# Optimization experiments

Hardware: AMD Instinct MI355X
Metric: run time of the kernel (lower is better)

## Reference

```python
import jax, jax.numpy as jnp
import numpy as np

N_ATOMS = 1_000_000
N_IN = 128
N_HID = 64
N_MOL = 25_000


def setup_inputs() -> dict:
    key = jax.random.key(0)
    k1, k2, k3, k4 = jax.random.split(key, 4)
    x = jax.random.normal(k1, (N_ATOMS, N_IN), dtype=jnp.float32)
    W1 = jax.random.normal(k2, (N_IN, N_HID), dtype=jnp.float32) * (1.0 / np.sqrt(N_IN))
    b1 = jnp.zeros((N_HID,), dtype=jnp.float32)
    W2 = jax.random.normal(k3, (N_HID, 1), dtype=jnp.float32) * (1.0 / np.sqrt(N_HID))
    b2 = jnp.zeros((1,), dtype=jnp.float32)
    idx_m = jnp.sort(jax.random.randint(k4, (N_ATOMS,), 0, N_MOL, dtype=jnp.int32))
    return {"x": x, "W1": W1, "b1": b1, "W2": W2, "b2": b2,
            "idx_m": idx_m, "num_segments": N_MOL}


def reference(x, W1, b1, W2, b2, idx_m, num_segments):
    # Atomwise MLP: Dense(silu) -> Dense(linear), per-atom output [N, 1]
    h = jax.nn.silu(x @ W1 + b1)            # [N, 64]
    y_atom = h @ W2 + b2                    # [N, 1]
    # scatter_add over molecule ids, then squeeze last dim
    y = jax.ops.segment_sum(y_atom, idx_m, num_segments=num_segments)  # [M, 1]
    y = jnp.squeeze(y, -1)                  # [M]
    return y
```

## Files before the change

### kernel.cpp

```cpp
#include <hip/hip_runtime.h>
#include <hip/hip_bf16.h>

typedef __attribute__((ext_vector_type(8))) short bf16x8;
typedef __attribute__((ext_vector_type(4))) short s16x4;
typedef __attribute__((ext_vector_type(4))) float f32x4;
typedef __attribute__((ext_vector_type(4))) int   i32x4;

#define N_IN  128
#define N_HID 64
#define LDS_PAD 8
#define TPB 256
#define WAVES_PER_BLOCK 4

static __device__ inline short f2bf(float f) {
    unsigned u = __float_as_uint(f);
    u += 0x7fffu + ((u >> 16) & 1u);
    return (short)(u >> 16);
}

static __device__ inline bf16x8 cvt8(f32x4 lo, f32x4 hi) {
    int i0, i1, i2, i3;
    asm("v_cvt_pk_bf16_f32 %0, %1, %2" : "=v"(i0) : "v"(lo[0]), "v"(lo[1]));
    asm("v_cvt_pk_bf16_f32 %0, %1, %2" : "=v"(i1) : "v"(lo[2]), "v"(lo[3]));
    asm("v_cvt_pk_bf16_f32 %0, %1, %2" : "=v"(i2) : "v"(hi[0]), "v"(hi[1]));
    asm("v_cvt_pk_bf16_f32 %0, %1, %2" : "=v"(i3) : "v"(hi[2]), "v"(hi[3]));
    i32x4 w = {i0, i1, i2, i3};
    return __builtin_bit_cast(bf16x8, w);
}


__global__ __launch_bounds__(TPB, 3)
void atomwise_mfma_kernel(const float* __restrict__ x,
                          const float* __restrict__ W1,
                          const float* __restrict__ b1,
                          const float* __restrict__ W2,
                          const float* __restrict__ b2,
                          const int*   __restrict__ idx_m,
                          float*       __restrict__ out,
                          int n_atoms)
{
    __shared__ short w1t[N_HID][N_IN + LDS_PAD];

    const int tid = threadIdx.x;

    for (int e = tid; e < N_IN * N_HID; e += TPB) {
        int k = e >> 6;
        int n = e & 63;
        w1t[n][k] = f2bf(W1[e]);
    }
    __syncthreads();

    const int lane = tid & 63;
    const int wv   = tid >> 6;
    const int l15  = lane & 15;
    const int g    = lane >> 4;

    bf16x8 bfrag[4][4];
    #pragma unroll
    for (int kt = 0; kt < 4; ++kt)
        #pragma unroll
        for (int nt = 0; nt < 4; ++nt) {
            const short* rp = &w1t[nt * 16 + l15][kt * 32 + g * 4];
            s16x4 q0 = *reinterpret_cast<const s16x4*>(rp);
            s16x4 q1 = *reinterpret_cast<const s16x4*>(rp + 16);
            bf16x8 b;
            b[0] = q0[0]; b[1] = q0[1]; b[2] = q0[2]; b[3] = q0[3];
            b[4] = q1[0]; b[5] = q1[1]; b[6] = q1[2]; b[7] = q1[3];
            bfrag[kt][nt] = b;
        }

    float bb[4], w2v[4];
    #pragma unroll
    for (int nt = 0; nt < 4; ++nt) {
        bb[nt]  = b1[nt * 16 + l15];
        w2v[nt] = W2[nt * 16 + l15];
    }
    const float b2v = b2[0];

    const int n_tiles = (n_atoms + 15) >> 4;
    const int n_waves = gridDim.x * WAVES_PER_BLOCK;
    int tile = blockIdx.x * WAVES_PER_BLOCK + wv;
    if (tile >= n_tiles) return;

    f32x4 xf[8];
    int mv;
    {
        int row  = tile * 16 + l15;
        int rowc = row < n_atoms ? row : (n_atoms - 1);
        const float* xp = x + (size_t)rowc * N_IN + g * 4;
        #pragma unroll
        for (int j = 0; j < 8; ++j)
            xf[j] = *reinterpret_cast<const f32x4*>(xp + j * 16);
        mv = idx_m[rowc];
    }

    while (true) {
        bf16x8 a[4];
        #pragma unroll
        for (int kt = 0; kt < 4; ++kt)
            a[kt] = cvt8(xf[2 * kt], xf[2 * kt + 1]);

        const int  ntile     = tile + n_waves;
        const bool have_next = ntile < n_tiles;
        int nmv = 0;
        if (have_next) {
            int row  = ntile * 16 + l15;
            int rowc = row < n_atoms ? row : (n_atoms - 1);
            const float* xp = x + (size_t)rowc * N_IN + g * 4;
            #pragma unroll
            for (int j = 0; j < 8; ++j)
                xf[j] = *reinterpret_cast<const f32x4*>(xp + j * 16);
            nmv = idx_m[rowc];
        }

        f32x4 acc[4] = {};
        #pragma unroll
        for (int kt = 0; kt < 4; ++kt)
            #pragma unroll
            for (int nt = 0; nt < 4; ++nt)
                acc[nt] = __builtin_amdgcn_mfma_f32_16x16x32_bf16(
                              a[kt], bfrag[kt][nt], acc[nt], 0, 0, 0);

        float p[4];
        #pragma unroll
        for (int j = 0; j < 4; ++j) {
            float s = 0.f;
            #pragma unroll
            for (int nt = 0; nt < 4; ++nt) {
                float z = acc[nt][j] + bb[nt];
                float e = __expf(-z);
                float h = z * __builtin_amdgcn_rcpf(1.f + e);
                s += h * w2v[nt];
            }
            p[j] = s;
        }

        const int  first = __shfl(mv, 0);
        const bool full  = (tile * 16 + 16) <= n_atoms;
        const bool uni   = full && (__all(mv == first) != 0);

        if (uni) {
            float s = p[0] + p[1] + p[2] + p[3];
            #pragma unroll
            for (int m = 1; m < 64; m <<= 1)
                s += __shfl_xor(s, m, 64);
            if (lane == 0)
                atomicAdd(&out[first], s + 16.0f * b2v);
        } else {
            int ia[4];
            #pragma unroll
            for (int j = 0; j < 4; ++j)
                ia[j] = __shfl(mv, g * 4 + j);
            #pragma unroll
            for (int m = 1; m < 16; m <<= 1) {
                #pragma unroll
                for (int j = 0; j < 4; ++j)
                    p[j] += __shfl_xor(p[j], m, 64);
            }
            if (l15 == 0) {
                #pragma unroll
                for (int j = 0; j < 4; ++j) {
                    int atom = tile * 16 + g * 4 + j;
                    if (atom < n_atoms)
                        atomicAdd(&out[ia[j]], p[j] + b2v);
                }
            }
        }

        if (!have_next) break;
        tile = ntile;
        mv   = nmv;
    }
}

extern "C" void kernel_launch(void* const* d_in, const int* in_sizes, int n_in,
                              void* d_out, int out_size, void* d_ws, size_t ws_size,
                              hipStream_t stream) {
    const float* x   = (const float*)d_in[0];
    const float* W1  = (const float*)d_in[1];
    const float* b1  = (const float*)d_in[2];
    const float* W2  = (const float*)d_in[3];
    const float* b2  = (const float*)d_in[4];
    const int*   idx = (const int*)d_in[5];

    const int n_atoms = in_sizes[0] / N_IN;
    float* out = (float*)d_out;

    hipMemsetAsync(d_out, 0, (size_t)out_size * sizeof(float), stream);

    const int blocks = 2048;
    atomwise_mfma_kernel<<<blocks, TPB, 0, stream>>>(
        x, W1, b1, W2, b2, idx, out, n_atoms);
}
```

Before: 113.2 us.

## Double-buffer x tile prefetch with two interleaved tiles per wave

Each wave now keeps two independent tiles in flight (A and B), prefetching the tile two steps ahead for each buffer, so more global loads are outstanding while MFMA and the epilogue run. The epilogue is factored into a helper. The launch-bounds occupancy hint drops from 3 to 2 to give room for the extra register buffers. This trades fewer resident waves for more memory-level parallelism per wave.

Measured after the change: 117.2 us. 3.6% more time.

```diff
diff --git a/kernel.cpp b/kernel.cpp
--- a/kernel.cpp
+++ b/kernel.cpp
@@ -28,8 +28,59 @@
     return __builtin_bit_cast(bf16x8, w);
 }
 
-
-__global__ __launch_bounds__(TPB, 3)
+static __device__ __forceinline__ void epilogue_store(
+    const f32x4* acc, const float* bb, const float* w2v, float b2v,
+    int tile, int mv, int lane, int l15, int g, int n_atoms,
+    float* __restrict__ out)
+{
+    float p[4];
+    #pragma unroll
+    for (int j = 0; j < 4; ++j) {
+        float s = 0.f;
+        #pragma unroll
+        for (int nt = 0; nt < 4; ++nt) {
+            float z = acc[nt][j] + bb[nt];
+            float e = __expf(-z);
+            float h = z * __builtin_amdgcn_rcpf(1.f + e);
+            s += h * w2v[nt];
+        }
+        p[j] = s;
+    }
+
+    const int  first = __shfl(mv, 0);
+    const bool full  = (tile * 16 + 16) <= n_atoms;
+    const bool uni   = full && (__all(mv == first) != 0);
+
+    if (uni) {
+        float s = p[0] + p[1] + p[2] + p[3];
+        #pragma unroll
+        for (int m = 1; m < 64; m <<= 1)
+            s += __shfl_xor(s, m, 64);
+        if (lane == 0)
+            atomicAdd(&out[first], s + 16.0f * b2v);
+    } else {
+        int ia[4];
+        #pragma unroll
+        for (int j = 0; j < 4; ++j)
+            ia[j] = __shfl(mv, g * 4 + j);
+        #pragma unroll
+        for (int m = 1; m < 16; m <<= 1) {
+            #pragma unroll
+            for (int j = 0; j < 4; ++j)
+                p[j] += __shfl_xor(p[j], m, 64);
+        }
+        if (l15 == 0) {
+            #pragma unroll
+            for (int j = 0; j < 4; ++j) {
+                int atom = tile * 16 + g * 4 + j;
+                if (atom < n_atoms)
+                    atomicAdd(&out[ia[j]], p[j] + b2v);
+            }
+        }
+    }
+}
+
+__global__ __launch_bounds__(TPB, 2)
 void atomwise_mfma_kernel(const float* __restrict__ x,
                           const float* __restrict__ W1,
                           const float* __restrict__ b1,
@@ -78,99 +129,81 @@
     const float b2v = b2[0];
 
     const int n_tiles = (n_atoms + 15) >> 4;
-    const int n_waves = gridDim.x * WAVES_PER_BLOCK;
-    int tile = blockIdx.x * WAVES_PER_BLOCK + wv;
-    if (tile >= n_tiles) return;
-
-    f32x4 xf[8];
-    int mv;
-    {
-        int row  = tile * 16 + l15;
-        int rowc = row < n_atoms ? row : (n_atoms - 1);
-        const float* xp = x + (size_t)rowc * N_IN + g * 4;
-        #pragma unroll
-        for (int j = 0; j < 8; ++j)
-            xf[j] = *reinterpret_cast<const f32x4*>(xp + j * 16);
-        mv = idx_m[rowc];
-    }
+    const int step    = gridDim.x * WAVES_PER_BLOCK;
+
+    int tA = blockIdx.x * WAVES_PER_BLOCK + wv;
+    if (tA >= n_tiles) return;
+    int  tB   = tA + step;
+    bool hasB = tB < n_tiles;
+
+#define LOADX(BUF, MVDST, TT) do {                                        \
+        int row_  = (TT) * 16 + l15;                                      \
+        int rowc_ = row_ < n_atoms ? row_ : (n_atoms - 1);                \
+        const float* xp_ = x + (size_t)rowc_ * N_IN + g * 4;              \
+        _Pragma("unroll")                                                 \
+        for (int j_ = 0; j_ < 8; ++j_)                                    \
+            BUF[j_] = *reinterpret_cast<const f32x4*>(xp_ + j_ * 16);     \
+        MVDST = idx_m[rowc_];                                             \
+    } while (0)
+
+    f32x4 xfA[8], xfB[8];
+    int mvA = 0, mvB = 0;
+    LOADX(xfA, mvA, tA);
+    if (hasB) LOADX(xfB, mvB, tB);
+
+    int  tA2 = 0, tB2 = 0, nmvA = 0, nmvB = 0;
+    bool hA2 = false, hB2 = false;
 
     while (true) {
-        bf16x8 a[4];
-        #pragma unroll
-        for (int kt = 0; kt < 4; ++kt)
-            a[kt] = cvt8(xf[2 * kt], xf[2 * kt + 1]);
-
-        const int  ntile     = tile + n_waves;
-        const bool have_next = ntile < n_tiles;
-        int nmv = 0;
-        if (have_next) {
-            int row  = ntile * 16 + l15;
-            int rowc = row < n_atoms ? row : (n_atoms - 1);
-            const float* xp = x + (size_t)rowc * N_IN + g * 4;
-            #pragma unroll
-            for (int j = 0; j < 8; ++j)
-                xf[j] = *reinterpret_cast<const f32x4*>(xp + j * 16);
-            nmv = idx_m[rowc];
-        }
-
-        f32x4 acc[4] = {};
-        #pragma unroll
-        for (int kt = 0; kt < 4; ++kt)
-            #pragma unroll
-            for (int nt = 0; nt < 4; ++nt)
-                acc[nt] = __builtin_amdgcn_mfma_f32_16x16x32_bf16(
-                              a[kt], bfrag[kt][nt], acc[nt], 0, 0, 0);
-
-        float p[4];
-        #pragma unroll
-        for (int j = 0; j < 4; ++j) {
-            float s = 0.f;
-            #pragma unroll
-            for (int nt = 0; nt < 4; ++nt) {
-                float z = acc[nt][j] + bb[nt];
-                float e = __expf(-z);
-                float h = z * __builtin_amdgcn_rcpf(1.f + e);
-                s += h * w2v[nt];
-            }
-            p[j] = s;
-        }
-
-        const int  first = __shfl(mv, 0);
-        const bool full  = (tile * 16 + 16) <= n_atoms;
-        const bool uni   = full && (__all(mv == first) != 0);
-
-        if (uni) {
-            float s = p[0] + p[1] + p[2] + p[3];
-            #pragma unroll
-            for (int m = 1; m < 64; m <<= 1)
-                s += __shfl_xor(s, m, 64);
-            if (lane == 0)
-                atomicAdd(&out[first], s + 16.0f * b2v);
-        } else {
-            int ia[4];
-            #pragma unroll
-            for (int j = 0; j < 4; ++j)
-                ia[j] = __shfl(mv, g * 4 + j);
-            #pragma unroll
-            for (int m = 1; m < 16; m <<= 1) {
+        {
+            bf16x8 a[4];
+            #pragma unroll
+            for (int kt = 0; kt < 4; ++kt)
+                a[kt] = cvt8(xfA[2 * kt], xfA[2 * kt + 1]);
+
+            tA2 = tA + 2 * step;
+            hA2 = tA2 < n_tiles;
+            if (hA2) LOADX(xfA, nmvA, tA2);
+
+            f32x4 acc[4] = {};
+            #pragma unroll
+            for (int kt = 0; kt < 4; ++kt)
                 #pragma unroll
-                for (int j = 0; j < 4; ++j)
-                    p[j] += __shfl_xor(p[j], m, 64);
-            }
-            if (l15 == 0) {
+                for (int nt = 0; nt < 4; ++nt)
+                    acc[nt] = __builtin_amdgcn_mfma_f32_16x16x32_bf16(
+                                  a[kt], bfrag[kt][nt], acc[nt], 0, 0, 0);
+
+            epilogue_store(acc, bb, w2v, b2v, tA, mvA, lane, l15, g, n_atoms, out);
+        }
+        if (!hasB) break;
+
+        {
+            bf16x8 a[4];
+            #pragma unroll
+            for (int kt = 0; kt < 4; ++kt)
+                a[kt] = cvt8(xfB[2 * kt], xfB[2 * kt + 1]);
+
+            tB2 = tB + 2 * step;
+            hB2 = tB2 < n_tiles;
+            if (hB2) LOADX(xfB, nmvB, tB2);
+
+            f32x4 acc[4] = {};
+            #pragma unroll
+            for (int kt = 0; kt < 4; ++kt)
                 #pragma unroll
-                for (int j = 0; j < 4; ++j) {
-                    int atom = tile * 16 + g * 4 + j;
-                    if (atom < n_atoms)
-                        atomicAdd(&out[ia[j]], p[j] + b2v);
-                }
-            }
-        }
-
-        if (!have_next) break;
-        tile = ntile;
-        mv   = nmv;
-    }
+                for (int nt = 0; nt < 4; ++nt)
+                    acc[nt] = __builtin_amdgcn_mfma_f32_16x16x32_bf16(
+                                  a[kt], bfrag[kt][nt], acc[nt], 0, 0, 0);
+
+            epilogue_store(acc, bb, w2v, b2v, tB, mvB, lane, l15, g, n_atoms, out);
+        }
+        if (!hA2) break;
+
+        tA = tA2; mvA = nmvA;
+        if (hB2) { tB = tB2; mvB = nmvB; }
+        hasB = hB2;
+    }
+#undef LOADX
 }
 
 extern "C" void kernel_launch(void* const* d_in, const int* in_sizes, int n_in,
```
